# Kernel optimization log

Measured on AMD Instinct MI355X. Metric: run time of the kernel, lower is better.

Reference implementation:

```python
import jax, jax.numpy as jnp
import numpy as np

TEMPORAL_WIDTH = 4  # hardcoded in GRUBlock


def causal_conv1d(x, w, b):
    """Depthwise causal temporal conv. x:[B,T,R], w:[4,R], b:[R].
    out[t] = sum_i w[i] * x[t - 3 + i] + b (zero left padding)."""
    T = x.shape[1]
    xp = jnp.pad(x, ((0, 0), (TEMPORAL_WIDTH - 1, 0), (0, 0)))
    y = b
    for i in range(TEMPORAL_WIDTH):  # tiny fixed loop over 4 taps
        y = y + w[i] * xp[:, i:i + T]
    return y


def linear_scan(a, b):
    """h_t = a_t * h_{t-1} + b_t with h_{-1}=0, via associative scan over time."""
    def comb(e1, e2):
        a1, b1 = e1
        a2, b2 = e2
        return a2 * a1, a2 * b1 + b2
    _, h = jax.lax.associative_scan(comb, (a, b), axis=1)
    return h


def setup_inputs() -> dict:
    key = jax.random.key(0)
    k1, k2, k3, k4 = jax.random.split(key, 4)
    B, T, H, R = 4, 8192, 1024, 1024
    x = jax.random.normal(k1, (B, T, H), dtype=jnp.float32)
    # lecun init: N(0, 1/sqrt(d_in)); torch Linear weight is [out, in]
    w_zh = jax.random.normal(k2, (2 * R, H), dtype=jnp.float32) / np.sqrt(H)
    w_out = jax.random.normal(k3, (H, R), dtype=jnp.float32) / np.sqrt(R)
    conv_w = jax.random.normal(k4, (TEMPORAL_WIDTH, R), dtype=jnp.float32) / np.sqrt(TEMPORAL_WIDTH)
    conv_b = jnp.zeros((R,), dtype=jnp.float32)
    return {"x": x, "w_zh": w_zh, "w_out": w_out, "conv_w": conv_w, "conv_b": conv_b}


def reference(x, w_zh, w_out, conv_w, conv_b):
    # residual causal conv
    x = x + causal_conv1d(x, conv_w, conv_b)
    # fused z/h projection: [B,T,H] @ [H,2R]
    zh = jnp.einsum('bth,rh->btr', x, w_zh)
    z, h = jnp.split(zh, 2, axis=-1)
    z = jax.nn.sigmoid(z)
    # GRU-style linear recurrence: h_t = (1-z_t) h_{t-1} + z_t h~_t
    h_o = linear_scan(1.0 - z, z * h)
    return jnp.einsum('btr,hr->bth', h_o, w_out)
```

## Files before the change

kernel.cpp:

```cpp
#include <hip/hip_runtime.h>

typedef __bf16 bf16x8 __attribute__((ext_vector_type(8)));
typedef __bf16 bf16x4 __attribute__((ext_vector_type(4)));
typedef float  f32x4  __attribute__((ext_vector_type(4)));
typedef float  f32x16 __attribute__((ext_vector_type(16)));

static constexpr int Bb = 4, T = 8192, H = 1024, R = 1024;
static constexpr int BT = Bb * T;
static constexpr int N1 = 2 * R;
static constexpr int CH = 128;
static constexpr int L  = T / CH;

__device__ __forceinline__ void g2lds16(const void* g, void* l) {
  __builtin_amdgcn_global_load_lds(
      (const __attribute__((address_space(1))) unsigned int*)g,
      (__attribute__((address_space(3))) unsigned int*)l, 16, 0, 0);
}

__global__ __launch_bounds__(256) void cast_f32_bf16(const float* __restrict__ in,
                                                     __bf16* __restrict__ out, int n4) {
  int i = blockIdx.x * 256 + threadIdx.x;
  if (i >= n4) return;
  const f32x4 v = *(const f32x4*)(in + (size_t)i * 4);
  bf16x4 o;
  o[0] = (__bf16)v[0]; o[1] = (__bf16)v[1]; o[2] = (__bf16)v[2]; o[3] = (__bf16)v[3];
  *(bf16x4*)(out + (size_t)i * 4) = o;
}

__global__ __launch_bounds__(256) void conv_residual_cast(const float* __restrict__ x,
                                                          const float* __restrict__ cw,
                                                          const float* __restrict__ cb,
                                                          __bf16* __restrict__ xc) {
  const int h  = threadIdx.x * 4;
  const int b  = blockIdx.y;
  const int t0 = blockIdx.x * 8;
  const f32x4 w0 = *(const f32x4*)(cw + 0 * H + h);
  const f32x4 w1 = *(const f32x4*)(cw + 1 * H + h);
  const f32x4 w2 = *(const f32x4*)(cw + 2 * H + h);
  const f32x4 w3 = *(const f32x4*)(cw + 3 * H + h);
  const f32x4 bias = *(const f32x4*)(cb + h);
  size_t base = ((size_t)b * T + t0) * H + h;
  f32x4 xm3, xm2, xm1;
  if (t0 >= 3) {
    xm3 = *(const f32x4*)(x + base - 3 * H);
    xm2 = *(const f32x4*)(x + base - 2 * H);
    xm1 = *(const f32x4*)(x + base - 1 * H);
  } else {
    xm3 = f32x4{0, 0, 0, 0}; xm2 = xm3; xm1 = xm3;
  }
#pragma unroll
  for (int tt = 0; tt < 8; ++tt) {
    const f32x4 x0 = *(const f32x4*)(x + base);
    const f32x4 acc = x0 + bias + w0 * xm3 + w1 * xm2 + w2 * xm1 + w3 * x0;
    bf16x4 o;
    o[0] = (__bf16)acc[0]; o[1] = (__bf16)acc[1]; o[2] = (__bf16)acc[2]; o[3] = (__bf16)acc[3];
    *(bf16x4*)(xc + base) = o;
    xm3 = xm2; xm2 = xm1; xm1 = x0;
    base += H;
  }
}


#define STG_A(buf, k0, ro) g2lds16(aBase + (size_t)(r + (ro)) * K + (k0), \
                                   &sA[buf][(w8 + (ro)) * 64])
#define STG_B(buf, k0, ro) g2lds16(bBase + (size_t)(rB + (ro)) * K + (k0), \
                                   &sB[buf][(w8B + (ro)) * 64])
#define STAGE_A02(buf, kt) do { const int k0_ = (kt) * 64; STG_A(buf, k0_, 0);  STG_A(buf, k0_, 128); } while (0)
#define STAGE_A13(buf, kt) do { const int k0_ = (kt) * 64; STG_A(buf, k0_, 64); STG_A(buf, k0_, 192); } while (0)
#define STAGE_BEV(buf, kt) do { const int k0_ = (kt) * 64; STG_B(buf, k0_, 0);  STG_B(buf, k0_, 128); } while (0)
#define STAGE_BOD(buf, kt) do { const int k0_ = (kt) * 64; STG_B(buf, k0_, 32); STG_B(buf, k0_, 160); } while (0)

#define RD_A(dst, MQ, SRC) do {                                                      \
    _Pragma("unroll") for (int m_ = 0; m_ < 2; ++m_) {                               \
      const int rt_ = aRowBase + (MQ) * 64 + m_ * 32;                                \
      _Pragma("unroll") for (int ks_ = 0; ks_ < 4; ++ks_)                            \
        dst[m_][ks_] = *(const bf16x8*)&(SRC)[rt_ * 64 + (((2 * ks_ + kb) ^ (rt_ & 7)) * 8)]; \
    } } while (0)

#define RD_B(dst, NQ, SRC) do {                                                      \
    const int rt_ = bRowBase + (NQ) * 32;                                            \
    _Pragma("unroll") for (int ks_ = 0; ks_ < 4; ++ks_)                              \
      dst[ks_] = *(const bf16x8*)&(SRC)[rt_ * 64 + (((2 * ks_ + kb) ^ (rt_ & 7)) * 8)]; \
  } while (0)

#define MFMA_CL(AF, BF, MQ, NQ) do {                                                 \
    __builtin_amdgcn_s_setprio(1);                                                   \
    _Pragma("unroll") for (int ks_ = 0; ks_ < 4; ++ks_)                              \
      _Pragma("unroll") for (int m_ = 0; m_ < 2; ++m_)                               \
        acc[(MQ) * 2 + m_][NQ] = __builtin_amdgcn_mfma_f32_32x32x16_bf16(            \
            AF[m_][ks_], BF[ks_], acc[(MQ) * 2 + m_][NQ], 0, 0, 0);                  \
    __builtin_amdgcn_s_setprio(0);                                                   \
  } while (0)

#define SB0 __builtin_amdgcn_sched_barrier(0)
#define BARRIER asm volatile("s_barrier" ::: "memory")
#define VMCNT4 asm volatile("s_waitcnt vmcnt(4)" ::: "memory")

#define TILE_BODY(KT, CI, NI) do {                                                   \
    const int kt1 = ((KT) + 1 < NT) ? (KT) + 1 : NT - 1;                             \
    const int kt2 = ((KT) + 2 < NT) ? (KT) + 2 : NT - 1;                             \
     RD_B(bfO, 1, sB[CI]); STAGE_A13(NI, kt1); SB0;                         \
    MFMA_CL(afA, bfE, 0, 0); BARRIER;                                                \
     RD_A(afB, 1, sA[CI]); STAGE_BOD(NI, kt1); SB0;                         \
    MFMA_CL(afA, bfO, 0, 1); VMCNT4; BARRIER;                                        \
     RD_A(afA, 0, sA[NI]); STAGE_BEV(CI, kt2); SB0;                         \
    MFMA_CL(afB, bfO, 1, 1); BARRIER;                                                \
     STAGE_A02(CI, kt2); SB0;                                               \
    MFMA_CL(afB, bfE, 1, 0); SB0;                                                    \
    RD_B(bfE, 0, sB[NI]); VMCNT4; BARRIER;                                           \
  } while (0)

template <typename OUT_T>
__global__ __launch_bounds__(512, 2) void gemm256(const __bf16* __restrict__ A,
                                                  const __bf16* __restrict__ Bm,
                                                  OUT_T* __restrict__ C,
                                                  int M, int N, int K, int nbx) {
  __shared__ __align__(16) __bf16 sA[2][256 * 64];
  __shared__ __align__(16) __bf16 sB[2][256 * 64];
  const int tid  = threadIdx.x;
  const int wave = tid >> 6;
  const int lane = tid & 63;
  const int wm = wave >> 2;
  const int wn = wave & 3;

  const int nwg = gridDim.x;
  int wg = blockIdx.x;
  wg = (wg & 7) * (nwg >> 3) + (wg >> 3);
  const int bm0 = (wg / nbx) * 256;
  const int bn0 = (wg % nbx) * 256;

  const int NT = K >> 6;

  const int r   = tid >> 3;
  const int sgc = (tid & 7) ^ (r & 7);
  const int rB  = r + (r & 32);
  const int w8  = wave * 8;
  const int w8B = w8 + (w8 & 32);
  const __bf16* aBase = A  + (size_t)bm0 * K + sgc * 8;
  const __bf16* bBase = Bm + (size_t)bn0 * K + sgc * 8;

  const int ln = lane & 31;
  const int kb = lane >> 5;
  const int aRowBase = wm * 128 + ln;
  const int bRowBase = wn * 64 + ln;

  f32x16 acc[4][2] = {};
  bf16x8 afA[2][4], afB[2][4], bfE[4], bfO[4];

  STAGE_BEV(0, 0);
  STAGE_A02(0, 0);
  STAGE_A13(0, 0);
  STAGE_BOD(0, 0);
  {
    const int k1 = NT > 1 ? 1 : 0;
    STAGE_BEV(1, k1);
    STAGE_A02(1, k1);
  }
  VMCNT4;
  BARRIER;
  RD_A(afA, 0, sA[0]);
  RD_B(bfE, 0, sB[0]);

  for (int kt = 0; kt < NT; kt += 2) {
    TILE_BODY(kt, 0, 1);
    TILE_BODY(kt + 1, 1, 0);
  }

  const int orow0 = bm0 + wm * 128;
  const int ocol0 = bn0 + wn * 64;
#pragma unroll
  for (int a = 0; a < 4; ++a)
#pragma unroll
    for (int j = 0; j < 2; ++j) {
      const int col = ocol0 + j * 32 + ln;
#pragma unroll
      for (int rr = 0; rr < 16; ++rr) {
        const int row = orow0 + a * 32 + (rr & 3) + 8 * (rr >> 2) + 4 * kb;
        C[(size_t)row * N + col] = (OUT_T)acc[a][j][rr];
      }
    }
}

__global__ __launch_bounds__(256) void scan_pass1(const __bf16* __restrict__ zh,
                                                  float* __restrict__ aggA,
                                                  float* __restrict__ aggB) {
  const int r = (blockIdx.x * 256 + threadIdx.x) * 4;
  const int c = blockIdx.y;
  const int b = blockIdx.z;
  size_t base = ((size_t)b * T + (size_t)c * L) * N1 + r;
  float Aacc[4] = {1.f, 1.f, 1.f, 1.f};
  float Bacc[4] = {0.f, 0.f, 0.f, 0.f};
#pragma unroll 4
  for (int t = 0; t < L; ++t) {
    const bf16x4 s4 = *(const bf16x4*)(zh + base);
    const bf16x4 h4 = *(const bf16x4*)(zh + base + R);
    base += N1;
#pragma unroll
    for (int j = 0; j < 4; ++j) {
      const float z = 1.f / (1.f + __expf(-(float)s4[j]));
      const float a = 1.f - z;
      Bacc[j] = a * Bacc[j] + z * (float)h4[j];
      Aacc[j] *= a;
    }
  }
  const size_t o = ((size_t)b * CH + c) * R + r;
  *(f32x4*)(aggA + o) = f32x4{Aacc[0], Aacc[1], Aacc[2], Aacc[3]};
  *(f32x4*)(aggB + o) = f32x4{Bacc[0], Bacc[1], Bacc[2], Bacc[3]};
}

__global__ __launch_bounds__(64) void scan_pass2(const float* __restrict__ aggA,
                                                 const float* __restrict__ aggB,
                                                 float* __restrict__ carry) {
  const int idx = blockIdx.x * 64 + threadIdx.x;
  const int b = idx >> 10;
  const int r = idx & (R - 1);
  float h = 0.f;
#pragma unroll 8
  for (int c = 0; c < CH; ++c) {
    const size_t o = ((size_t)b * CH + c) * R + r;
    carry[o] = h;
    h = aggA[o] * h + aggB[o];
  }
}

__global__ __launch_bounds__(256) void scan_pass3(const __bf16* __restrict__ zh,
                                                  const float* __restrict__ carry,
                                                  __bf16* __restrict__ ho) {
  const int r = (blockIdx.x * 256 + threadIdx.x) * 4;
  const int c = blockIdx.y;
  const int b = blockIdx.z;
  size_t base  = ((size_t)b * T + (size_t)c * L) * N1 + r;
  size_t obase = ((size_t)b * T + (size_t)c * L) * R + r;
  float h[4];
  const f32x4 cv = *(const f32x4*)(carry + ((size_t)b * CH + c) * R + r);
  h[0] = cv[0]; h[1] = cv[1]; h[2] = cv[2]; h[3] = cv[3];
#pragma unroll 4
  for (int t = 0; t < L; ++t) {
    const bf16x4 s4 = *(const bf16x4*)(zh + base);
    const bf16x4 h4 = *(const bf16x4*)(zh + base + R);
    base += N1;
    bf16x4 o;
#pragma unroll
    for (int j = 0; j < 4; ++j) {
      const float z = 1.f / (1.f + __expf(-(float)s4[j]));
      h[j] = (1.f - z) * h[j] + z * (float)h4[j];
      o[j] = (__bf16)h[j];
    }
    *(bf16x4*)(ho + obase) = o;
    obase += R;
  }
}

extern "C" void kernel_launch(void* const* d_in, const int* in_sizes, int n_in,
                              void* d_out, int out_size, void* d_ws, size_t ws_size,
                              hipStream_t stream) {
  const float* x      = (const float*)d_in[0];
  const float* w_zh   = (const float*)d_in[1];
  const float* w_out  = (const float*)d_in[2];
  const float* conv_w = (const float*)d_in[3];
  const float* conv_b = (const float*)d_in[4];
  float* out = (float*)d_out;

  char* ws = (char*)d_ws;
  size_t off = 0;
  __bf16* wzh_b  = (__bf16*)(ws + off); off += (size_t)N1 * H * 2;
  __bf16* wout_b = (__bf16*)(ws + off); off += (size_t)H * R * 2;
  __bf16* xc     = (__bf16*)(ws + off); off += (size_t)BT * H * 2;
  __bf16* zh     = (__bf16*)(ws + off); off += (size_t)BT * N1 * 2;
  float*  carry  = (float*)(ws + off);  off += (size_t)Bb * CH * R * 4;
  float*  aggA   = (float*)wzh_b;
  float*  aggB   = (float*)((char*)wzh_b + (size_t)Bb * CH * R * 4);
  __bf16* ho = xc;

  cast_f32_bf16<<<(N1 * H / 4 + 255) / 256, 256, 0, stream>>>(w_zh, wzh_b, N1 * H / 4);
  cast_f32_bf16<<<(H * R / 4 + 255) / 256, 256, 0, stream>>>(w_out, wout_b, H * R / 4);
  conv_residual_cast<<<dim3(T / 8, Bb), 256, 0, stream>>>(x, conv_w, conv_b, xc);
  gemm256<__bf16><<<(BT / 256) * (N1 / 256), 512, 0, stream>>>(xc, wzh_b, zh, BT, N1, H, N1 / 256);
  scan_pass1<<<dim3(R / 4 / 256, CH, Bb), 256, 0, stream>>>(zh, aggA, aggB);
  scan_pass2<<<Bb * R / 64, 64, 0, stream>>>(aggA, aggB, carry);
  scan_pass3<<<dim3(R / 4 / 256, CH, Bb), 256, 0, stream>>>(zh, carry, ho);
  gemm256<float><<<(BT / 256) * (H / 256), 512, 0, stream>>>(ho, wout_b, out, BT, H, R, H / 256);
}
```

Measured before the change: 552.7 us.

## Switch GEMM to 16x16x32 MFMA tiles and restructure the LDS pipeline

```diff
diff --git a/kernel.cpp b/kernel.cpp
--- a/kernel.cpp
+++ b/kernel.cpp
@@ -3,7 +3,6 @@
 typedef __bf16 bf16x8 __attribute__((ext_vector_type(8)));
 typedef __bf16 bf16x4 __attribute__((ext_vector_type(4)));
 typedef float  f32x4  __attribute__((ext_vector_type(4)));
-typedef float  f32x16 __attribute__((ext_vector_type(16)));
 
 static constexpr int Bb = 4, T = 8192, H = 1024, R = 1024;
 static constexpr int BT = Bb * T;
@@ -71,43 +70,63 @@
 #define STAGE_BOD(buf, kt) do { const int k0_ = (kt) * 64; STG_B(buf, k0_, 32); STG_B(buf, k0_, 160); } while (0)
 
 #define RD_A(dst, MQ, SRC) do {                                                      \
-    _Pragma("unroll") for (int m_ = 0; m_ < 2; ++m_) {                               \
-      const int rt_ = aRowBase + (MQ) * 64 + m_ * 32;                                \
-      _Pragma("unroll") for (int ks_ = 0; ks_ < 4; ++ks_)                            \
-        dst[m_][ks_] = *(const bf16x8*)&(SRC)[rt_ * 64 + (((2 * ks_ + kb) ^ (rt_ & 7)) * 8)]; \
+    _Pragma("unroll") for (int i_ = 0; i_ < 4; ++i_) {                               \
+      const int rt_ = aRowBase + (MQ) * 64 + i_ * 16;                                \
+      _Pragma("unroll") for (int ks_ = 0; ks_ < 2; ++ks_)                            \
+        dst[i_][ks_] = *(const bf16x8*)&(SRC)[rt_ * 64 + (((ks_ * 4 + kg) ^ (rt_ & 7)) * 8)]; \
     } } while (0)
 
 #define RD_B(dst, NQ, SRC) do {                                                      \
-    const int rt_ = bRowBase + (NQ) * 32;                                            \
-    _Pragma("unroll") for (int ks_ = 0; ks_ < 4; ++ks_)                              \
-      dst[ks_] = *(const bf16x8*)&(SRC)[rt_ * 64 + (((2 * ks_ + kb) ^ (rt_ & 7)) * 8)]; \
-  } while (0)
+    _Pragma("unroll") for (int j_ = 0; j_ < 2; ++j_) {                               \
+      const int rt_ = bRowBase + (NQ) * 32 + j_ * 16;                                \
+      _Pragma("unroll") for (int ks_ = 0; ks_ < 2; ++ks_)                            \
+        dst[j_][ks_] = *(const bf16x8*)&(SRC)[rt_ * 64 + (((ks_ * 4 + kg) ^ (rt_ & 7)) * 8)]; \
+    } } while (0)
 
 #define MFMA_CL(AF, BF, MQ, NQ) do {                                                 \
     __builtin_amdgcn_s_setprio(1);                                                   \
-    _Pragma("unroll") for (int ks_ = 0; ks_ < 4; ++ks_)                              \
-      _Pragma("unroll") for (int m_ = 0; m_ < 2; ++m_)                               \
-        acc[(MQ) * 2 + m_][NQ] = __builtin_amdgcn_mfma_f32_32x32x16_bf16(            \
-            AF[m_][ks_], BF[ks_], acc[(MQ) * 2 + m_][NQ], 0, 0, 0);                  \
+    _Pragma("unroll") for (int i_ = 0; i_ < 4; ++i_)                                 \
+      _Pragma("unroll") for (int j_ = 0; j_ < 2; ++j_)                               \
+        _Pragma("unroll") for (int ks_ = 0; ks_ < 2; ++ks_)                          \
+          acc[(MQ) * 4 + i_][(NQ) * 2 + j_] = __builtin_amdgcn_mfma_f32_16x16x32_bf16( \
+              AF[i_][ks_], BF[j_][ks_], acc[(MQ) * 4 + i_][(NQ) * 2 + j_], 0, 0, 0); \
     __builtin_amdgcn_s_setprio(0);                                                   \
   } while (0)
 
 #define SB0 __builtin_amdgcn_sched_barrier(0)
 #define BARRIER asm volatile("s_barrier" ::: "memory")
 #define VMCNT4 asm volatile("s_waitcnt vmcnt(4)" ::: "memory")
-
-#define TILE_BODY(KT, CI, NI) do {                                                   \
-    const int kt1 = ((KT) + 1 < NT) ? (KT) + 1 : NT - 1;                             \
-    const int kt2 = ((KT) + 2 < NT) ? (KT) + 2 : NT - 1;                             \
-     RD_B(bfO, 1, sB[CI]); STAGE_A13(NI, kt1); SB0;                         \
-    MFMA_CL(afA, bfE, 0, 0); BARRIER;                                                \
-     RD_A(afB, 1, sA[CI]); STAGE_BOD(NI, kt1); SB0;                         \
-    MFMA_CL(afA, bfO, 0, 1); VMCNT4; BARRIER;                                        \
-     RD_A(afA, 0, sA[NI]); STAGE_BEV(CI, kt2); SB0;                         \
-    MFMA_CL(afB, bfO, 1, 1); BARRIER;                                                \
-     STAGE_A02(CI, kt2); SB0;                                               \
-    MFMA_CL(afB, bfE, 1, 0); SB0;                                                    \
-    RD_B(bfE, 0, sB[NI]); VMCNT4; BARRIER;                                           \
+#define LGKM0  asm volatile("s_waitcnt lgkmcnt(0)" ::: "memory")
+#define LGKM8  asm volatile("s_waitcnt lgkmcnt(8)" ::: "memory")
+
+#define TILE_BODY(KT, CI, NI) do {                                        \
+    const int kt1 = ((KT) + 1 < NT) ? (KT) + 1 : NT - 1;                  \
+    const int kt2 = ((KT) + 2 < NT) ? (KT) + 2 : NT - 1;                  \
+                                                                 \
+    RD_A(afA, 0, sA[CI]); RD_B(bfE, 0, sB[CI]);                           \
+    STAGE_BOD(NI, kt1);                                                   \
+    LGKM8;                                                                \
+    BARRIER; LGKM0; SB0;                                                  \
+    MFMA_CL(afA, bfE, 0, 0);                                              \
+    BARRIER;                                                              \
+                                                                 \
+    RD_B(bfO, 1, sB[CI]);                                                 \
+    STAGE_A13(NI, kt1);                                                   \
+    BARRIER; LGKM0; SB0;                                                  \
+    MFMA_CL(afA, bfO, 0, 1);                                              \
+    BARRIER;                                                              \
+                                                                 \
+    RD_A(afB, 1, sA[CI]);                                                 \
+    STAGE_A02(CI, kt2);                                                   \
+    BARRIER; LGKM0; SB0;                                                  \
+    MFMA_CL(afB, bfO, 1, 1);                                              \
+    BARRIER;                                                              \
+                                                                 \
+    STAGE_BEV(CI, kt2);                                                   \
+    BARRIER; SB0;                                                         \
+    MFMA_CL(afB, bfE, 1, 0);                                              \
+    VMCNT4;                                                               \
+    BARRIER;                                                              \
   } while (0)
 
 template <typename OUT_T>
@@ -139,45 +158,41 @@
   const __bf16* aBase = A  + (size_t)bm0 * K + sgc * 8;
   const __bf16* bBase = Bm + (size_t)bn0 * K + sgc * 8;
 
-  const int ln = lane & 31;
-  const int kb = lane >> 5;
-  const int aRowBase = wm * 128 + ln;
-  const int bRowBase = wn * 64 + ln;
-
-  f32x16 acc[4][2] = {};
-  bf16x8 afA[2][4], afB[2][4], bfE[4], bfO[4];
-
+  const int l15 = lane & 15;
+  const int kg  = lane >> 4;
+  const int aRowBase = wm * 128 + l15;
+  const int bRowBase = wn * 64 + l15;
+
+  f32x4 acc[8][4] = {};
+  bf16x8 afA[4][2], afB[4][2], bfE[2][2], bfO[2][2];
+
+  STAGE_A02(0, 0);
   STAGE_BEV(0, 0);
-  STAGE_A02(0, 0);
+  STAGE_BOD(0, 0);
   STAGE_A13(0, 0);
-  STAGE_BOD(0, 0);
   {
     const int k1 = NT > 1 ? 1 : 0;
+    STAGE_A02(1, k1);
     STAGE_BEV(1, k1);
-    STAGE_A02(1, k1);
   }
   VMCNT4;
   BARRIER;
-  RD_A(afA, 0, sA[0]);
-  RD_B(bfE, 0, sB[0]);
 
   for (int kt = 0; kt < NT; kt += 2) {
     TILE_BODY(kt, 0, 1);
     TILE_BODY(kt + 1, 1, 0);
   }
 
-  const int orow0 = bm0 + wm * 128;
-  const int ocol0 = bn0 + wn * 64;
-#pragma unroll
-  for (int a = 0; a < 4; ++a)
-#pragma unroll
-    for (int j = 0; j < 2; ++j) {
-      const int col = ocol0 + j * 32 + ln;
-#pragma unroll
-      for (int rr = 0; rr < 16; ++rr) {
-        const int row = orow0 + a * 32 + (rr & 3) + 8 * (rr >> 2) + 4 * kb;
-        C[(size_t)row * N + col] = (OUT_T)acc[a][j][rr];
-      }
+  const int orow0 = bm0 + wm * 128 + kg * 4;
+  const int ocol0 = bn0 + wn * 64 + l15;
+#pragma unroll
+  for (int mi = 0; mi < 8; ++mi)
+#pragma unroll
+    for (int nj = 0; nj < 4; ++nj) {
+      const size_t rbase = (size_t)(orow0 + mi * 16);
+#pragma unroll
+      for (int rr = 0; rr < 4; ++rr)
+        C[(rbase + rr) * N + (ocol0 + nj * 16)] = (OUT_T)acc[mi][nj][rr];
     }
 }
 
```

Measured after the change: 538.4 us. 2.6% less time.
